# Optimization experiments

Measured on AMD Instinct MI355X. Metric: run time of the kernel, lower is better.

The kernel has to match this reference:

```python
import jax, jax.numpy as jnp
import numpy as np

DIM = 1024
HEADS = 16
HEAD_DIM = DIM // HEADS
HIDDEN = int(DIM * 4.0)
EPS = 1e-5


def layernorm(x, w, b):
    m = jnp.mean(x, axis=-1, keepdims=True)
    v = jnp.var(x, axis=-1, keepdims=True)
    return (x - m) * jax.lax.rsqrt(v + EPS) * w + b


def apply_rope(t, pos):
    # t: [B, H, S, D], pos: [B, S] int
    half = t.shape[-1] // 2
    inv_freq = 1.0 / (10000.0 ** (jnp.arange(half, dtype=jnp.float32) / half))
    ang = pos.astype(jnp.float32)[:, None, :, None] * inv_freq  # [B,1,S,half]
    cos = jnp.cos(ang)
    sin = jnp.sin(ang)
    t1, t2 = t[..., :half], t[..., half:]
    return jnp.concatenate([t1 * cos - t2 * sin, t2 * cos + t1 * sin], axis=-1)


def setup_inputs() -> dict:
    key = jax.random.key(0)
    ks = jax.random.split(key, 10)
    B, S = 2, 2048
    x = jax.random.normal(ks[0], (B, S, DIM), dtype=jnp.float32)
    pos = jnp.sort(jax.random.randint(ks[1], (B, S), 0, 2048), axis=-1).astype(jnp.int32)
    def lin(k, fi, fo):
        return jax.random.normal(k, (fi, fo), dtype=jnp.float32) / np.sqrt(fi)
    return {
        "x": x,
        "pos": pos,
        "ln1_w": jnp.ones((DIM,), jnp.float32),
        "ln1_b": jnp.zeros((DIM,), jnp.float32),
        "qkv_w": lin(ks[2], DIM, 3 * DIM),
        "qkv_b": jnp.zeros((3 * DIM,), jnp.float32),
        "o_w": lin(ks[3], DIM, DIM),
        "o_b": jnp.zeros((DIM,), jnp.float32),
        "ln2_w": jnp.ones((DIM,), jnp.float32),
        "ln2_b": jnp.zeros((DIM,), jnp.float32),
        "mlp_w1": lin(ks[4], DIM, HIDDEN),
        "mlp_b1": jnp.zeros((HIDDEN,), jnp.float32),
        "mlp_w2": lin(ks[5], HIDDEN, DIM),
        "mlp_b2": jnp.zeros((DIM,), jnp.float32),
    }


def reference(x, pos, ln1_w, ln1_b, qkv_w, qkv_b, o_w, o_b, ln2_w, ln2_b, mlp_w1, mlp_b1, mlp_w2, mlp_b2):
    B, S, C = x.shape
    scale = HEAD_DIM ** -0.5
    xn = layernorm(x, ln1_w, ln1_b)
    qkv = (xn @ qkv_w + qkv_b).reshape(B, S, 3, HEADS, HEAD_DIM)
    qkv = jnp.transpose(qkv, (2, 0, 3, 1, 4))  # [3,B,H,S,D]
    q, k, v = qkv[0], qkv[1], qkv[2]
    q = apply_rope(q, pos)
    k = apply_rope(k, pos)
    scores = jnp.einsum("bhsd,bhtd->bhst", q, k) * scale
    probs = jax.nn.softmax(scores, axis=-1)
    attn = jnp.einsum("bhst,bhtd->bhsd", probs, v)
    attn = jnp.transpose(attn, (0, 2, 1, 3)).reshape(B, S, C)
    x = x + attn @ o_w + o_b
    xn2 = layernorm(x, ln2_w, ln2_b)
    h = jax.nn.gelu(xn2 @ mlp_w1 + mlp_b1, approximate=False)
    x = x + h @ mlp_w2 + mlp_b2
    return x
```

## Files before the change

kernel.cpp:

```cpp
#include <hip/hip_runtime.h>
#include <hip/hip_bf16.h>
#include <math.h>

#define DIMC 1024
#define HEADS 16
#define HD 64
#define HIDDEN 4096
#define BATCH 2
#define SEQ 2048
#define TOK (BATCH*SEQ)

typedef unsigned short u16;
typedef __attribute__((ext_vector_type(8))) short short8;
typedef __attribute__((ext_vector_type(4))) float f32x4;

__device__ __forceinline__ u16 f2bf(float f) {
  unsigned u = __float_as_uint(f);
  u += 0x7fff + ((u >> 16) & 1);
  return (u16)(u >> 16);
}
__device__ __forceinline__ float bf2f(u16 h) {
  return __uint_as_float(((unsigned)h) << 16);
}

__device__ __forceinline__ void gl_lds16(const void* g, void* l) {
  __builtin_amdgcn_global_load_lds(
      (__attribute__((address_space(1))) void*)g,
      (__attribute__((address_space(3))) void*)l, 16, 0, 0);
}

__device__ __forceinline__ const short8* lds_row128(const u16* base, int row, int chunk) {
  return (const short8*)((const char*)base + row * 128 + (((chunk) ^ (row & 7)) << 4));
}

__global__ __launch_bounds__(256) void ln_kernel(
    const float* __restrict__ x, const float* __restrict__ w,
    const float* __restrict__ b, u16* __restrict__ out)
{
  int row = blockIdx.x, tid = threadIdx.x;
  const float4* xr = (const float4*)(x + (size_t)row * DIMC);
  float4 v = xr[tid];
  float s = v.x + v.y + v.z + v.w;
  float s2 = v.x*v.x + v.y*v.y + v.z*v.z + v.w*v.w;
  for (int off = 32; off > 0; off >>= 1) {
    s  += __shfl_down(s, off);
    s2 += __shfl_down(s2, off);
  }
  __shared__ float red[8];
  int lane = tid & 63, wv = tid >> 6;
  if (lane == 0) { red[wv] = s; red[4 + wv] = s2; }
  __syncthreads();
  float S  = red[0] + red[1] + red[2] + red[3];
  float S2 = red[4] + red[5] + red[6] + red[7];
  float mean = S * (1.f / DIMC);
  float var  = S2 * (1.f / DIMC) - mean * mean;
  float inv  = rsqrtf(var + 1e-5f);
  int base = tid * 4;
  float vv[4] = {v.x, v.y, v.z, v.w};
#pragma unroll
  for (int j = 0; j < 4; ++j)
    out[(size_t)row * DIMC + base + j] = f2bf((vv[j] - mean) * inv * w[base + j] + b[base + j]);
}

__global__ __launch_bounds__(256) void transpose_cast(
    const float* __restrict__ W, u16* __restrict__ Wt, int K, int N)
{
  __shared__ float t[32][33];
  int n0 = blockIdx.x * 32, k0 = blockIdx.y * 32;
  for (int r = threadIdx.y; r < 32; r += 8)
    t[r][threadIdx.x] = W[(size_t)(k0 + r) * N + n0 + threadIdx.x];
  __syncthreads();
  for (int r = threadIdx.y; r < 32; r += 8)
    Wt[(size_t)(n0 + r) * K + k0 + threadIdx.x] = f2bf(t[threadIdx.x][r]);
}

template<int EPI>
__global__ __launch_bounds__(256) void gemm_bt(
    const u16* __restrict__ A, const u16* __restrict__ Bt,
    const float* __restrict__ bias, const float* __restrict__ res,
    u16* __restrict__ outb, float* __restrict__ outf,
    int M, int N, int K)
{
  __shared__ u16 As[2][128 * 32];
  __shared__ u16 Bs[2][128 * 32];
  int tid = threadIdx.x;
  int lane = tid & 63, w = tid >> 6;
  int m0 = blockIdx.x * 128, n0 = blockIdx.y * 128;
  int wr = w >> 1, wc = w & 1;
  f32x4 acc[4][4] = {};

  int trow = tid >> 2, tk = (tid & 3) * 8;
  const u16* ga = A  + (size_t)(m0 + trow) * K + tk;
  const u16* gb = Bt + (size_t)(n0 + trow) * K + tk;
  int rofs = lane & 15, kofs = (lane >> 4) * 8;
  int nt = K >> 5;

#define G_STAGE(BUF) do { \
    gl_lds16(ga, &As[BUF][tid * 8]); \
    gl_lds16(ga + (size_t)64 * K, &As[BUF][tid * 8 + 2048]); \
    gl_lds16(gb, &Bs[BUF][tid * 8]); \
    gl_lds16(gb + (size_t)64 * K, &Bs[BUF][tid * 8 + 2048]); \
    ga += 32; gb += 32; } while (0)

#define G_COMPUTE(BUF) do { \
    short8 af[4], bfr[4]; \
    _Pragma("unroll") for (int mm = 0; mm < 4; ++mm) \
      af[mm] = *(const short8*)&As[BUF][(wr * 64 + mm * 16 + rofs) * 32 + kofs]; \
    _Pragma("unroll") for (int nn = 0; nn < 4; ++nn) \
      bfr[nn] = *(const short8*)&Bs[BUF][(wc * 64 + nn * 16 + rofs) * 32 + kofs]; \
    _Pragma("unroll") for (int mm = 0; mm < 4; ++mm) \
      _Pragma("unroll") for (int nn = 0; nn < 4; ++nn) \
        acc[mm][nn] = __builtin_amdgcn_mfma_f32_16x16x32_bf16(af[mm], bfr[nn], acc[mm][nn], 0, 0, 0); \
    } while (0)

  G_STAGE(0);
  __syncthreads();
  for (int t = 0; t < nt; t += 2) {
    if (t + 1 < nt) G_STAGE(1);
    G_COMPUTE(0);
    __syncthreads();
    if (t + 2 < nt) G_STAGE(0);
    G_COMPUTE(1);
    __syncthreads();
  }
#undef G_STAGE
#undef G_COMPUTE

  int crow0 = m0 + wr * 64 + (lane >> 4) * 4;
  int ccol0 = n0 + wc * 64 + rofs;
#pragma unroll
  for (int nn = 0; nn < 4; ++nn) {
    int col = ccol0 + nn * 16;
    float bv = bias[col];
#pragma unroll
    for (int mm = 0; mm < 4; ++mm) {
#pragma unroll
      for (int r = 0; r < 4; ++r) {
        int row = crow0 + mm * 16 + r;
        size_t idx = (size_t)row * N + col;
        float v = acc[mm][nn][r] + bv;
        if (EPI == 0) outb[idx] = f2bf(v);
        else if (EPI == 1) outb[idx] = f2bf(0.5f * v * (1.f + erff(v * 0.70710678118f)));
        else outf[idx] = v + res[idx];
      }
    }
  }
}

__global__ __launch_bounds__(256) void rope_split(
    const u16* __restrict__ qkv, const int* __restrict__ pos,
    u16* __restrict__ Q, u16* __restrict__ Kk, u16* __restrict__ Vt)
{
  int st = blockIdx.x, bh = blockIdx.y;
  int b = bh >> 4, hh = bh & 15;
  int s0 = st * 64;
  int tid = threadIdx.x;
  __shared__ u16 vtile[64][72];

  for (int i = tid; i < 64 * 32; i += 256) {
    int sl = i >> 5, dp = i & 31;
    int s = s0 + sl;
    float p = (float)pos[b * SEQ + s];
    float freq = exp2f((float)dp * -0.4152410118609203f);
    float ang = p * freq;
    float sn, c;
    __sincosf(ang, &sn, &c);
    const u16* qr = qkv + (size_t)(b * SEQ + s) * 3072 + hh * 64;
    float q1 = bf2f(qr[dp]),        q2 = bf2f(qr[dp + 32]);
    float k1 = bf2f(qr[1024 + dp]), k2 = bf2f(qr[1024 + dp + 32]);
    size_t ob = ((size_t)bh * SEQ + s) * HD;
    const float QS = 0.18033688011112042f;
    Q[ob + dp]       = f2bf((q1 * c - q2 * sn) * QS);
    Q[ob + dp + 32]  = f2bf((q2 * c + q1 * sn) * QS);
    Kk[ob + dp]      = f2bf(k1 * c - k2 * sn);
    Kk[ob + dp + 32] = f2bf(k2 * c + k1 * sn);
  }
  for (int i = tid; i < 64 * 64; i += 256) {
    int sl = i >> 6, d = i & 63;
    vtile[d][sl] = qkv[(size_t)(b * SEQ + s0 + sl) * 3072 + 2048 + hh * 64 + d];
  }
  __syncthreads();
  for (int i = tid; i < 64 * 64; i += 256) {
    int d = i >> 6, sl = i & 63;
    Vt[((size_t)bh * HD + d) * SEQ + s0 + sl] = vtile[d][sl];
  }
}

__global__ __launch_bounds__(256) void attn_kernel(
    const u16* __restrict__ Q, const u16* __restrict__ K,
    const u16* __restrict__ Vt, u16* __restrict__ O)
{
  __shared__ u16 Ks[2][64 * 64];
  __shared__ u16 Vs[2][64 * 64];
  __shared__ u16 Ps[4 * 16 * 64];
  int qt = blockIdx.x, bh = blockIdx.y;
  int b = bh >> 4, hh = bh & 15;
  const u16* Qp = Q + ((size_t)bh * SEQ + qt * 64) * HD;
  const u16* Kp = K + (size_t)bh * SEQ * HD;
  const u16* Vp = Vt + (size_t)bh * HD * SEQ;
  int tid = threadIdx.x, lane = tid & 63, w = tid >> 6;
  int rofs = lane & 15, q4 = lane >> 4;
  int kofs = q4 * 8;

  short8 aq0 = *(const short8*)&Qp[(w * 16 + rofs) * HD + kofs];
  short8 aq1 = *(const short8*)&Qp[(w * 16 + rofs) * HD + 32 + kofs];

  short8 ones;
#pragma unroll
  for (int j = 0; j < 8; ++j) ones[j] = (short)0x3F80;

  f32x4 o[4] = {};
  f32x4 lsum = {};

  int srow = tid >> 3;
  int sg0 = ((tid & 7) ^ (srow & 7)) * 8;
  u16* pw = &Ps[w * 16 * 64];

#define A_STAGE(BUF, T0) do { \
    gl_lds16(Kp + (size_t)((T0) + srow) * HD + sg0, &Ks[BUF][tid * 8]); \
    gl_lds16(Kp + (size_t)((T0) + 32 + srow) * HD + sg0, &Ks[BUF][tid * 8 + 2048]); \
    gl_lds16(Vp + (size_t)srow * SEQ + (T0) + sg0, &Vs[BUF][tid * 8]); \
    gl_lds16(Vp + (size_t)(32 + srow) * SEQ + (T0) + sg0, &Vs[BUF][tid * 8 + 2048]); \
  } while (0)

  auto tile = [&](const u16* KsB, const u16* VsB) {
    f32x4 s[4] = {};
#pragma unroll
    for (int n = 0; n < 4; ++n) {
      int krow = n * 16 + rofs;
      short8 bk0 = *lds_row128(KsB, krow, q4);
      short8 bk1 = *lds_row128(KsB, krow, 4 + q4);
      s[n] = __builtin_amdgcn_mfma_f32_16x16x32_bf16(aq0, bk0, s[n], 0, 0, 0);
      s[n] = __builtin_amdgcn_mfma_f32_16x16x32_bf16(aq1, bk1, s[n], 0, 0, 0);
    }
#pragma unroll
    for (int n = 0; n < 4; ++n)
#pragma unroll
      for (int r = 0; r < 4; ++r) {
        int prow = q4 * 4 + r;
        int pbyte = (n * 16 + rofs) * 2;
        float p = __builtin_amdgcn_exp2f(s[n][r]);
        *(u16*)((char*)pw + prow * 128 + (pbyte ^ ((prow & 7) << 4))) = f2bf(p);
      }
    short8 pa0 = *lds_row128(pw, rofs, q4);
    short8 pa1 = *lds_row128(pw, rofs, 4 + q4);
    lsum = __builtin_amdgcn_mfma_f32_16x16x32_bf16(pa0, ones, lsum, 0, 0, 0);
    lsum = __builtin_amdgcn_mfma_f32_16x16x32_bf16(pa1, ones, lsum, 0, 0, 0);
#pragma unroll
    for (int n = 0; n < 4; ++n) {
      int vrow = n * 16 + rofs;
      short8 bv0 = *lds_row128(VsB, vrow, q4);
      short8 bv1 = *lds_row128(VsB, vrow, 4 + q4);
      o[n] = __builtin_amdgcn_mfma_f32_16x16x32_bf16(pa0, bv0, o[n], 0, 0, 0);
      o[n] = __builtin_amdgcn_mfma_f32_16x16x32_bf16(pa1, bv1, o[n], 0, 0, 0);
    }
  };

  A_STAGE(0, 0);
  __syncthreads();
  for (int t0 = 0; t0 < SEQ; t0 += 128) {
    if (t0 + 64 < SEQ) A_STAGE(1, t0 + 64);
    tile(Ks[0], Vs[0]);
    __syncthreads();
    if (t0 + 128 < SEQ) A_STAGE(0, t0 + 128);
    tile(Ks[1], Vs[1]);
    __syncthreads();
  }
#undef A_STAGE

#pragma unroll
  for (int r = 0; r < 4; ++r) {
    float inv = 1.f / lsum[r];
    int sq = qt * 64 + w * 16 + q4 * 4 + r;
#pragma unroll
    for (int n = 0; n < 4; ++n) {
      int col = hh * HD + n * 16 + rofs;
      O[((size_t)b * SEQ + sq) * DIMC + col] = f2bf(o[n][r] * inv);
    }
  }
}

extern "C" void kernel_launch(void* const* d_in, const int* in_sizes, int n_in,
                              void* d_out, int out_size, void* d_ws, size_t ws_size,
                              hipStream_t stream) {
  const float* x     = (const float*)d_in[0];
  const int*   pos   = (const int*)  d_in[1];
  const float* ln1_w = (const float*)d_in[2];
  const float* ln1_b = (const float*)d_in[3];
  const float* qkv_w = (const float*)d_in[4];
  const float* qkv_b = (const float*)d_in[5];
  const float* o_w   = (const float*)d_in[6];
  const float* o_b   = (const float*)d_in[7];
  const float* ln2_w = (const float*)d_in[8];
  const float* ln2_b = (const float*)d_in[9];
  const float* w1    = (const float*)d_in[10];
  const float* b1    = (const float*)d_in[11];
  const float* w2    = (const float*)d_in[12];
  const float* b2    = (const float*)d_in[13];
  float* out = (float*)d_out;

  char* ws = (char*)d_ws;
  u16* WqkvT = (u16*)(ws + 0);
  u16* WoT   = (u16*)(ws + 6291456);
  u16* W1T   = (u16*)(ws + 8388608);
  u16* W2T   = (u16*)(ws + 16777216);
  u16* xn    = (u16*)(ws + 25165824);
  u16* qkvbf = (u16*)(ws + 33554432);
  u16* Qb    = (u16*)(ws + 58720256);
  u16* Kb    = (u16*)(ws + 67108864);
  u16* Vtb   = (u16*)(ws + 75497472);
  u16* attnb = (u16*)(ws + 83886080);
  u16* hbuf  = (u16*)(ws + 25165824);
  float* x2  = (float*)(ws + 58720256);
  u16* xn2   = (u16*)(ws + 75497472);

  transpose_cast<<<dim3(3072/32, 1024/32), dim3(32, 8), 0, stream>>>(qkv_w, WqkvT, 1024, 3072);
  transpose_cast<<<dim3(1024/32, 1024/32), dim3(32, 8), 0, stream>>>(o_w,  WoT,  1024, 1024);
  transpose_cast<<<dim3(4096/32, 1024/32), dim3(32, 8), 0, stream>>>(w1,   W1T,  1024, 4096);
  transpose_cast<<<dim3(1024/32, 4096/32), dim3(32, 8), 0, stream>>>(w2,   W2T,  4096, 1024);

  ln_kernel<<<TOK, 256, 0, stream>>>(x, ln1_w, ln1_b, xn);
  gemm_bt<0><<<dim3(32, 24), 256, 0, stream>>>(xn, WqkvT, qkv_b, nullptr, qkvbf, nullptr, 4096, 3072, 1024);
  rope_split<<<dim3(32, 32), 256, 0, stream>>>(qkvbf, pos, Qb, Kb, Vtb);
  attn_kernel<<<dim3(32, 32), 256, 0, stream>>>(Qb, Kb, Vtb, attnb);
  gemm_bt<2><<<dim3(32, 8), 256, 0, stream>>>(attnb, WoT, o_b, x, nullptr, x2, 4096, 1024, 1024);
  ln_kernel<<<TOK, 256, 0, stream>>>(x2, ln2_w, ln2_b, xn2);
  gemm_bt<1><<<dim3(32, 32), 256, 0, stream>>>(xn2, W1T, b1, nullptr, hbuf, nullptr, 4096, 4096, 1024);
  gemm_bt<2><<<dim3(32, 8), 256, 0, stream>>>(hbuf, W2T, b2, x2, nullptr, out, 4096, 1024, 4096);
}
```

Measured before the change: 300.2 us.

## Triple-buffer GEMM LDS with XOR swizzle and explicit vmcnt waits

The bf16 MFMA GEMM moves from a double-buffered LDS pipeline to a three-stage ring buffer. It uses explicit s_waitcnt vmcnt counts and raw s_barrier calls so global-to-LDS loads stay in flight across two iterations. The LDS layout is XOR-swizzled on 16-byte chunks to cut bank conflicts on the short8 fragment reads. The block-index mapping is also swapped so consecutive blocks share the same A rows, and the launch grids change to match. This adds LDS usage (48KB), which may lower occupancy, and it relies on hand-counted vmcnt values being correct.

```diff
diff --git a/kernel.cpp b/kernel.cpp
--- a/kernel.cpp
+++ b/kernel.cpp
@@ -81,47 +81,59 @@
     u16* __restrict__ outb, float* __restrict__ outf,
     int M, int N, int K)
 {
-  __shared__ u16 As[2][128 * 32];
-  __shared__ u16 Bs[2][128 * 32];
+  __shared__ u16 As[3][128 * 32];
+  __shared__ u16 Bs[3][128 * 32];
   int tid = threadIdx.x;
   int lane = tid & 63, w = tid >> 6;
-  int m0 = blockIdx.x * 128, n0 = blockIdx.y * 128;
+  int m0 = blockIdx.y * 128, n0 = blockIdx.x * 128;
   int wr = w >> 1, wc = w & 1;
   f32x4 acc[4][4] = {};
 
-  int trow = tid >> 2, tk = (tid & 3) * 8;
+  int trow = tid >> 2;
+  int tk = (((tid & 3) ^ ((tid >> 3) & 3)) * 8);
   const u16* ga = A  + (size_t)(m0 + trow) * K + tk;
   const u16* gb = Bt + (size_t)(n0 + trow) * K + tk;
-  int rofs = lane & 15, kofs = (lane >> 4) * 8;
+  int rofs = lane & 15;
+  int ach = (((lane >> 4) ^ ((rofs >> 1) & 3)) << 4);
   int nt = K >> 5;
 
-#define G_STAGE(BUF) do { \
-    gl_lds16(ga, &As[BUF][tid * 8]); \
-    gl_lds16(ga + (size_t)64 * K, &As[BUF][tid * 8 + 2048]); \
-    gl_lds16(gb, &Bs[BUF][tid * 8]); \
-    gl_lds16(gb + (size_t)64 * K, &Bs[BUF][tid * 8 + 2048]); \
+  u16 *a0 = As[0], *a1 = As[1], *a2 = As[2];
+  u16 *b0 = Bs[0], *b1 = Bs[1], *b2 = Bs[2];
+
+#define G_STAGE(AB, BB) do { \
+    gl_lds16(ga, (AB) + tid * 8); \
+    gl_lds16(ga + (size_t)64 * K, (AB) + tid * 8 + 2048); \
+    gl_lds16(gb, (BB) + tid * 8); \
+    gl_lds16(gb + (size_t)64 * K, (BB) + tid * 8 + 2048); \
     ga += 32; gb += 32; } while (0)
 
-#define G_COMPUTE(BUF) do { \
+#define G_COMPUTE(AB, BB) do { \
     short8 af[4], bfr[4]; \
     _Pragma("unroll") for (int mm = 0; mm < 4; ++mm) \
-      af[mm] = *(const short8*)&As[BUF][(wr * 64 + mm * 16 + rofs) * 32 + kofs]; \
+      af[mm] = *(const short8*)((const char*)(AB) + (wr * 64 + mm * 16 + rofs) * 64 + ach); \
     _Pragma("unroll") for (int nn = 0; nn < 4; ++nn) \
-      bfr[nn] = *(const short8*)&Bs[BUF][(wc * 64 + nn * 16 + rofs) * 32 + kofs]; \
+      bfr[nn] = *(const short8*)((const char*)(BB) + (wc * 64 + nn * 16 + rofs) * 64 + ach); \
     _Pragma("unroll") for (int mm = 0; mm < 4; ++mm) \
       _Pragma("unroll") for (int nn = 0; nn < 4; ++nn) \
         acc[mm][nn] = __builtin_amdgcn_mfma_f32_16x16x32_bf16(af[mm], bfr[nn], acc[mm][nn], 0, 0, 0); \
     } while (0)
 
-  G_STAGE(0);
-  __syncthreads();
-  for (int t = 0; t < nt; t += 2) {
-    if (t + 1 < nt) G_STAGE(1);
-    G_COMPUTE(0);
-    __syncthreads();
-    if (t + 2 < nt) G_STAGE(0);
-    G_COMPUTE(1);
-    __syncthreads();
+  G_STAGE(a0, b0);
+  G_STAGE(a1, b1);
+  for (int t = 0; t < nt; ++t) {
+    if (t + 2 < nt) {
+      G_STAGE(a2, b2);
+      asm volatile("s_waitcnt vmcnt(8)" ::: "memory");
+    } else if (t + 1 < nt) {
+      asm volatile("s_waitcnt vmcnt(4)" ::: "memory");
+    } else {
+      asm volatile("s_waitcnt vmcnt(0)" ::: "memory");
+    }
+    __builtin_amdgcn_s_barrier();
+    G_COMPUTE(a0, b0);
+    __builtin_amdgcn_s_barrier();
+    u16* ta = a0; a0 = a1; a1 = a2; a2 = ta;
+    u16* tb = b0; b0 = b1; b1 = b2; b2 = tb;
   }
 #undef G_STAGE
 #undef G_COMPUTE
@@ -320,11 +332,11 @@
   transpose_cast<<<dim3(1024/32, 4096/32), dim3(32, 8), 0, stream>>>(w2,   W2T,  4096, 1024);
 
   ln_kernel<<<TOK, 256, 0, stream>>>(x, ln1_w, ln1_b, xn);
-  gemm_bt<0><<<dim3(32, 24), 256, 0, stream>>>(xn, WqkvT, qkv_b, nullptr, qkvbf, nullptr, 4096, 3072, 1024);
+  gemm_bt<0><<<dim3(24, 32), 256, 0, stream>>>(xn, WqkvT, qkv_b, nullptr, qkvbf, nullptr, 4096, 3072, 1024);
   rope_split<<<dim3(32, 32), 256, 0, stream>>>(qkvbf, pos, Qb, Kb, Vtb);
   attn_kernel<<<dim3(32, 32), 256, 0, stream>>>(Qb, Kb, Vtb, attnb);
-  gemm_bt<2><<<dim3(32, 8), 256, 0, stream>>>(attnb, WoT, o_b, x, nullptr, x2, 4096, 1024, 1024);
+  gemm_bt<2><<<dim3(8, 32), 256, 0, stream>>>(attnb, WoT, o_b, x, nullptr, x2, 4096, 1024, 1024);
   ln_kernel<<<TOK, 256, 0, stream>>>(x2, ln2_w, ln2_b, xn2);
   gemm_bt<1><<<dim3(32, 32), 256, 0, stream>>>(xn2, W1T, b1, nullptr, hbuf, nullptr, 4096, 4096, 1024);
-  gemm_bt<2><<<dim3(32, 8), 256, 0, stream>>>(hbuf, W2T, b2, x2, nullptr, out, 4096, 1024, 4096);
-}
+  gemm_bt<2><<<dim3(8, 32), 256, 0, stream>>>(hbuf, W2T, b2, x2, nullptr, out, 4096, 1024, 4096);
+}
```

Result: no change. 302.6 us (+0.8%).

## Swizzle GEMM LDS layout, stage epilogues through LDS, and reorder block grid

Applied to the files above, without the earlier changes.

Applies an XOR swizzle to the 16-byte chunks of the GEMM shared-memory tiles, on both the global-to-LDS load side and the MFMA fragment read side, to cut LDS bank conflicts. GEMM and attention epilogues now write results into shared memory first and then store them with coalesced 16-byte vector writes, replacing scattered 2-byte and 4-byte stores. The residual add uses float4 loads. The grid is swapped so blockIdx.x walks N tiles, which lets neighbouring blocks share A rows. The cost is extra LDS round-trips and barriers in the epilogue, and the f32 path is split into two passes because of LDS size.

```diff
diff --git a/kernel.cpp b/kernel.cpp
--- a/kernel.cpp
+++ b/kernel.cpp
@@ -81,33 +81,36 @@
     u16* __restrict__ outb, float* __restrict__ outf,
     int M, int N, int K)
 {
-  __shared__ u16 As[2][128 * 32];
-  __shared__ u16 Bs[2][128 * 32];
+  __shared__ u16 shm[16384];
+  u16* As[2] = { shm,        shm + 4096 };
+  u16* Bs[2] = { shm + 8192, shm + 12288 };
   int tid = threadIdx.x;
   int lane = tid & 63, w = tid >> 6;
-  int m0 = blockIdx.x * 128, n0 = blockIdx.y * 128;
+  int m0 = blockIdx.y * 128, n0 = blockIdx.x * 128;
   int wr = w >> 1, wc = w & 1;
   f32x4 acc[4][4] = {};
 
-  int trow = tid >> 2, tk = (tid & 3) * 8;
+  int trow = tid >> 2;
+  int tk = (((tid & 3) ^ ((tid >> 3) & 3)) * 8);
   const u16* ga = A  + (size_t)(m0 + trow) * K + tk;
   const u16* gb = Bt + (size_t)(n0 + trow) * K + tk;
-  int rofs = lane & 15, kofs = (lane >> 4) * 8;
+  int rofs = lane & 15, q4 = lane >> 4;
+  int ach = ((q4 ^ ((rofs >> 1) & 3)) << 4);
   int nt = K >> 5;
 
 #define G_STAGE(BUF) do { \
-    gl_lds16(ga, &As[BUF][tid * 8]); \
-    gl_lds16(ga + (size_t)64 * K, &As[BUF][tid * 8 + 2048]); \
-    gl_lds16(gb, &Bs[BUF][tid * 8]); \
-    gl_lds16(gb + (size_t)64 * K, &Bs[BUF][tid * 8 + 2048]); \
+    gl_lds16(ga, As[BUF] + tid * 8); \
+    gl_lds16(ga + (size_t)64 * K, As[BUF] + tid * 8 + 2048); \
+    gl_lds16(gb, Bs[BUF] + tid * 8); \
+    gl_lds16(gb + (size_t)64 * K, Bs[BUF] + tid * 8 + 2048); \
     ga += 32; gb += 32; } while (0)
 
 #define G_COMPUTE(BUF) do { \
     short8 af[4], bfr[4]; \
     _Pragma("unroll") for (int mm = 0; mm < 4; ++mm) \
-      af[mm] = *(const short8*)&As[BUF][(wr * 64 + mm * 16 + rofs) * 32 + kofs]; \
+      af[mm] = *(const short8*)((const char*)As[BUF] + (wr * 64 + mm * 16 + rofs) * 64 + ach); \
     _Pragma("unroll") for (int nn = 0; nn < 4; ++nn) \
-      bfr[nn] = *(const short8*)&Bs[BUF][(wc * 64 + nn * 16 + rofs) * 32 + kofs]; \
+      bfr[nn] = *(const short8*)((const char*)Bs[BUF] + (wc * 64 + nn * 16 + rofs) * 64 + ach); \
     _Pragma("unroll") for (int mm = 0; mm < 4; ++mm) \
       _Pragma("unroll") for (int nn = 0; nn < 4; ++nn) \
         acc[mm][nn] = __builtin_amdgcn_mfma_f32_16x16x32_bf16(af[mm], bfr[nn], acc[mm][nn], 0, 0, 0); \
@@ -126,23 +129,53 @@
 #undef G_STAGE
 #undef G_COMPUTE
 
-  int crow0 = m0 + wr * 64 + (lane >> 4) * 4;
-  int ccol0 = n0 + wc * 64 + rofs;
-#pragma unroll
-  for (int nn = 0; nn < 4; ++nn) {
-    int col = ccol0 + nn * 16;
-    float bv = bias[col];
-#pragma unroll
-    for (int mm = 0; mm < 4; ++mm) {
-#pragma unroll
-      for (int r = 0; r < 4; ++r) {
-        int row = crow0 + mm * 16 + r;
-        size_t idx = (size_t)row * N + col;
-        float v = acc[mm][nn][r] + bv;
-        if (EPI == 0) outb[idx] = f2bf(v);
-        else if (EPI == 1) outb[idx] = f2bf(0.5f * v * (1.f + erff(v * 0.70710678118f)));
-        else outf[idx] = v + res[idx];
+  if (EPI == 0 || EPI == 1) {
+    u16* C = shm;
+#pragma unroll
+    for (int nn = 0; nn < 4; ++nn) {
+      int ccol = wc * 64 + nn * 16 + rofs;
+      float bv = bias[n0 + ccol];
+#pragma unroll
+      for (int mm = 0; mm < 4; ++mm)
+#pragma unroll
+        for (int r = 0; r < 4; ++r) {
+          int crow = wr * 64 + mm * 16 + q4 * 4 + r;
+          float v = acc[mm][nn][r] + bv;
+          if (EPI == 1) v = 0.5f * v * (1.f + erff(v * 0.70710678118f));
+          C[crow * 128 + ccol] = f2bf(v);
+        }
+    }
+    __syncthreads();
+    for (int c = tid; c < 2048; c += 256) {
+      int row = c >> 4, off = (c & 15) * 8;
+      *(short8*)(outb + (size_t)(m0 + row) * N + n0 + off) = *(const short8*)&C[row * 128 + off];
+    }
+  } else {
+    float* Cf = (float*)shm;
+#pragma unroll
+    for (int p = 0; p < 2; ++p) {
+      if (wr == p) {
+#pragma unroll
+        for (int nn = 0; nn < 4; ++nn) {
+          int ccol = wc * 64 + nn * 16 + rofs;
+          float bv = bias[n0 + ccol];
+#pragma unroll
+          for (int mm = 0; mm < 4; ++mm)
+#pragma unroll
+            for (int r = 0; r < 4; ++r)
+              Cf[(mm * 16 + q4 * 4 + r) * 128 + ccol] = acc[mm][nn][r] + bv;
+        }
       }
+      __syncthreads();
+      for (int c = tid; c < 2048; c += 256) {
+        int row = c >> 5, off = (c & 31) * 4;
+        size_t idx = (size_t)(m0 + p * 64 + row) * N + n0 + off;
+        float4 rv = *(const float4*)(res + idx);
+        float4 cv = *(const float4*)&Cf[row * 128 + off];
+        cv.x += rv.x; cv.y += rv.y; cv.z += rv.z; cv.w += rv.w;
+        *(float4*)(outf + idx) = cv;
+      }
+      __syncthreads();
     }
   }
 }
@@ -271,12 +304,16 @@
 #pragma unroll
   for (int r = 0; r < 4; ++r) {
     float inv = 1.f / lsum[r];
-    int sq = qt * 64 + w * 16 + q4 * 4 + r;
-#pragma unroll
-    for (int n = 0; n < 4; ++n) {
-      int col = hh * HD + n * 16 + rofs;
-      O[((size_t)b * SEQ + sq) * DIMC + col] = f2bf(o[n][r] * inv);
-    }
+    int lrow = w * 16 + q4 * 4 + r;
+#pragma unroll
+    for (int n = 0; n < 4; ++n)
+      Ps[lrow * 64 + n * 16 + rofs] = f2bf(o[n][r] * inv);
+  }
+  __syncthreads();
+  for (int c = tid; c < 512; c += 256) {
+    int row = c >> 3, off = (c & 7) * 8;
+    int sq = qt * 64 + row;
+    *(short8*)(O + ((size_t)b * SEQ + sq) * DIMC + hh * 64 + off) = *(const short8*)&Ps[row * 64 + off];
   }
 }
 
@@ -320,11 +357,11 @@
   transpose_cast<<<dim3(1024/32, 4096/32), dim3(32, 8), 0, stream>>>(w2,   W2T,  4096, 1024);
 
   ln_kernel<<<TOK, 256, 0, stream>>>(x, ln1_w, ln1_b, xn);
-  gemm_bt<0><<<dim3(32, 24), 256, 0, stream>>>(xn, WqkvT, qkv_b, nullptr, qkvbf, nullptr, 4096, 3072, 1024);
+  gemm_bt<0><<<dim3(24, 32), 256, 0, stream>>>(xn, WqkvT, qkv_b, nullptr, qkvbf, nullptr, 4096, 3072, 1024);
   rope_split<<<dim3(32, 32), 256, 0, stream>>>(qkvbf, pos, Qb, Kb, Vtb);
   attn_kernel<<<dim3(32, 32), 256, 0, stream>>>(Qb, Kb, Vtb, attnb);
-  gemm_bt<2><<<dim3(32, 8), 256, 0, stream>>>(attnb, WoT, o_b, x, nullptr, x2, 4096, 1024, 1024);
+  gemm_bt<2><<<dim3(8, 32), 256, 0, stream>>>(attnb, WoT, o_b, x, nullptr, x2, 4096, 1024, 1024);
   ln_kernel<<<TOK, 256, 0, stream>>>(x2, ln2_w, ln2_b, xn2);
   gemm_bt<1><<<dim3(32, 32), 256, 0, stream>>>(xn2, W1T, b1, nullptr, hbuf, nullptr, 4096, 4096, 1024);
-  gemm_bt<2><<<dim3(32, 8), 256, 0, stream>>>(hbuf, W2T, b2, x2, nullptr, out, 4096, 1024, 4096);
-}
+  gemm_bt<2><<<dim3(8, 32), 256, 0, stream>>>(hbuf, W2T, b2, x2, nullptr, out, 4096, 1024, 4096);
+}
```

New measurement: 290.6 us. -3.2%, faster.
